# Performance work log

Hardware: AMD Instinct MI355X
Metric: run time of the kernel (lower is better)

The kernel has to match this reference:

```python
import jax, jax.numpy as jnp
import numpy as np

N_NODES = 30000
N_EDGES = 480000
N_GRAPHS = 500
D_IN = 78


def gcn_conv(x, W, b, src, dst, n_nodes):
    """PyG GCNConv: add self-loops, sym-normalize, linear then aggregate, bias after."""
    xw = x @ W  # [N, d_out]
    deg = jnp.zeros((n_nodes,), x.dtype).at[dst].add(1.0) + 1.0  # +1 self-loop
    dinv = jax.lax.rsqrt(deg)
    norm = dinv[src] * dinv[dst]  # [E]
    msg = xw[src] * norm[:, None]  # [E, d_out] edge gather
    out = jnp.zeros_like(xw).at[dst].add(msg)  # scatter-add to dst
    out = out + xw * (dinv * dinv)[:, None]  # self-loop contribution
    return out + b


def setup_inputs() -> dict:
    key = jax.random.key(0)
    ks = jax.random.split(key, 16)
    x = jax.random.normal(ks[0], (N_NODES, D_IN), dtype=jnp.float32)
    edge_index = jax.random.randint(ks[1], (2, N_EDGES), 0, N_NODES, dtype=jnp.int32)
    batch = jnp.sort(jax.random.randint(ks[2], (N_NODES,), 0, N_GRAPHS, dtype=jnp.int32))

    def lin(k, fi, fo):
        s = 1.0 / np.sqrt(fi)
        k1, k2 = jax.random.split(k)
        W = jax.random.uniform(k1, (fi, fo), jnp.float32, -s, s)
        b = jax.random.uniform(k2, (fo,), jnp.float32, -s, s)
        return W, b

    W1, b1 = lin(ks[3], D_IN, D_IN)
    W2, b2 = lin(ks[4], D_IN, D_IN * 2)
    W3, b3 = lin(ks[5], D_IN * 2, D_IN * 4)
    Wf1, bf1 = lin(ks[6], D_IN * 4, 1024)
    Wf2, bf2 = lin(ks[7], 1024, 128)
    return {"x": x, "edge_index": edge_index, "batch": batch,
            "W1": W1, "b1": b1, "W2": W2, "b2": b2, "W3": W3, "b3": b3,
            "Wf1": Wf1, "bf1": bf1, "Wf2": Wf2, "bf2": bf2}


def reference(x, edge_index, batch, W1, b1, W2, b2, W3, b3, Wf1, bf1, Wf2, bf2):
    src, dst = edge_index[0], edge_index[1]
    n = x.shape[0]
    h = jax.nn.relu(gcn_conv(x, W1, b1, src, dst, n))
    h = jax.nn.relu(gcn_conv(h, W2, b2, src, dst, n))
    h = jax.nn.relu(gcn_conv(h, W3, b3, src, dst, n))
    # global max pool over graphs
    pooled = jax.ops.segment_max(h, batch, num_segments=N_GRAPHS)  # [G, 312]
    pooled = jnp.where(jnp.isfinite(pooled), pooled, 0.0)  # guard empty segments
    out = jax.nn.relu(pooled @ Wf1 + bf1)
    out = out @ Wf2 + bf2  # dropout is identity in eval mode
    return out
```

## Files before the change

### kernel.cpp

```cpp
#include <hip/hip_runtime.h>

#define NODES  30000
#define EDGES  480000
#define GRAPHS 500
#define MPAD   30016
#define NB     118

typedef __bf16 bf16x8 __attribute__((ext_vector_type(8)));
typedef float  f32x4  __attribute__((ext_vector_type(4)));

__device__ __forceinline__ float4 f4add(float4 a, float4 b) {
    a.x += b.x; a.y += b.y; a.z += b.z; a.w += b.w; return a;
}
__device__ __forceinline__ float4 f4max(float4 a, float4 b) {
    a.x = fmaxf(a.x, b.x); a.y = fmaxf(a.y, b.y);
    a.z = fmaxf(a.z, b.z); a.w = fmaxf(a.w, b.w); return a;
}

__device__ __forceinline__ void split_f32(float a, unsigned short& hi, unsigned short& lo) {
    unsigned int u = __float_as_uint(a);
    unsigned int rh = (u + 0x7fffu + ((u >> 16) & 1u)) & 0xffff0000u;
    hi = (unsigned short)(rh >> 16);
    float l = a - __uint_as_float(rh);
    unsigned int ul = __float_as_uint(l);
    lo = (unsigned short)((ul + 0x7fffu + ((ul >> 16) & 1u)) >> 16);
}

__device__ __forceinline__ void gload_lds16(const void* g, void* l) {
    __builtin_amdgcn_global_load_lds(
        (__attribute__((address_space(1))) void*)g,
        (__attribute__((address_space(3))) void*)l, 16, 0, 0);
}

__global__ __launch_bounds__(256) void prep_kernel(
    const float* __restrict__ W1, const float* __restrict__ W2, const float* __restrict__ W3,
    unsigned short* __restrict__ h1, unsigned short* __restrict__ l1,
    unsigned short* __restrict__ h2, unsigned short* __restrict__ l2,
    unsigned short* __restrict__ h3, unsigned short* __restrict__ l3,
    const int* __restrict__ dst, int* __restrict__ cnt)
{
    int b = blockIdx.x, t = threadIdx.x;
    if (b < 640) {
        const float* W; unsigned short *oh, *ol; int n, K, N, Kp;
        if (b < 128)      { W = W1; oh = h1; ol = l1; n = b;       K = 78;  N = 78;  Kp = 96;  }
        else if (b < 320) { W = W2; oh = h2; ol = l2; n = b - 128; K = 78;  N = 156; Kp = 96;  }
        else              { W = W3; oh = h3; ol = l3; n = b - 320; K = 156; N = 312; Kp = 160; }
        if (t < Kp) {
            float v = (n < N && t < K) ? W[(size_t)t * N + n] : 0.0f;
            unsigned short h, l;
            split_f32(v, h, l);
            oh[(size_t)n * Kp + t] = h;
            ol[(size_t)n * Kp + t] = l;
        }
    } else {
        int i = (b - 640) * 256 + t;
        if (i < EDGES) atomicAdd(&cnt[dst[i]], 1);
    }
}

__global__ __launch_bounds__(256) void scan_bsum_kernel(const int* __restrict__ cnt,
                                                        int* __restrict__ bsum, int n) {
    __shared__ int buf[256];
    int t = threadIdx.x;
    int i = blockIdx.x * 256 + t;
    buf[t] = (i < n) ? cnt[i] : 0;
    __syncthreads();
    for (int ofs = 128; ofs > 0; ofs >>= 1) {
        if (t < ofs) buf[t] += buf[t + ofs];
        __syncthreads();
    }
    if (t == 0) bsum[blockIdx.x] = buf[0];
}

__global__ __launch_bounds__(128) void scan_top_kernel(const int* __restrict__ bsum,
                                                       int* __restrict__ boff) {
    __shared__ int buf[128];
    int t = threadIdx.x;
    int own = (t < NB) ? bsum[t] : 0;
    buf[t] = own;
    __syncthreads();
    for (int ofs = 1; ofs < 128; ofs <<= 1) {
        int v = (t >= ofs) ? buf[t - ofs] : 0;
        __syncthreads();
        buf[t] += v;
        __syncthreads();
    }
    if (t < NB) boff[t] = buf[t] - own;
}

__global__ __launch_bounds__(256) void scan_apply_kernel(const int* __restrict__ cnt,
                                                         const int* __restrict__ boff,
                                                         int* __restrict__ rowstart,
                                                         int* __restrict__ cursor,
                                                         float* __restrict__ dinv, int n) {
    __shared__ int buf[256];
    int t = threadIdx.x;
    int i = blockIdx.x * 256 + t;
    int own = (i < n) ? cnt[i] : 0;
    buf[t] = own;
    __syncthreads();
    for (int ofs = 1; ofs < 256; ofs <<= 1) {
        int v = (t >= ofs) ? buf[t - ofs] : 0;
        __syncthreads();
        buf[t] += v;
        __syncthreads();
    }
    if (i < n) {
        rowstart[i] = boff[blockIdx.x] + buf[t] - own;
        cursor[i] = 0;
        dinv[i] = rsqrtf((float)own + 1.0f);
    }
}

__global__ __launch_bounds__(256) void fill_prescale_kernel(
    const int* __restrict__ src, const int* __restrict__ dst,
    const int* __restrict__ rowstart, int* __restrict__ cursor, int* __restrict__ csr_src,
    const float* __restrict__ X, const float* __restrict__ dinv, float* __restrict__ Xs)
{
    int b = blockIdx.x, t = threadIdx.x;
    if (b < 1875) {
        int i = b * 256 + t;
        if (i < EDGES) {
            int d = dst[i];
            int pos = atomicAdd(&cursor[d], 1);
            csr_src[rowstart[d] + pos] = src[i];
        }
    } else {
        int i = (b - 1875) * 256 + t;
        if (i < NODES * 80) {
            int node = i / 80;
            int c = i - node * 80;
            Xs[i] = (c < 78) ? X[node * 78 + c] * dinv[node] : 0.0f;
        }
    }
}

template <int DV, int KQ>
__global__ __launch_bounds__(256) void agg_split_v4(
    const float* __restrict__ Xs, const int* __restrict__ rowstart,
    const int* __restrict__ cnt, const int* __restrict__ csr_src,
    const float* __restrict__ dinv,
    unsigned short* __restrict__ ohi, unsigned short* __restrict__ olo)
{
    constexpr int EPI = 64 / DV;
    constexpr int Kp = KQ * 4;
    int node = blockIdx.x * 4 + (threadIdx.x >> 6);
    int lane = threadIdx.x & 63;
    int sub = lane / DV;
    int c4 = lane - sub * DV;
    const float4* X4 = (const float4*)Xs;

    float4 accs[4] = {{0,0,0,0},{0,0,0,0},{0,0,0,0},{0,0,0,0}};
    int s = rowstart[node];
    int e = s + cnt[node];

    if (sub < EPI) {
        if (sub == 0) accs[0] = X4[(size_t)node * DV + c4];
        int j = s;
        for (; j + 12 * EPI <= e; j += 12 * EPI) {
            int idx[12];
            #pragma unroll
            for (int u = 0; u < 12; u++) idx[u] = csr_src[j + u * EPI + sub];
            float4 xv[12];
            #pragma unroll
            for (int u = 0; u < 12; u++) xv[u] = X4[(size_t)idx[u] * DV + c4];
            #pragma unroll
            for (int u = 0; u < 12; u++) accs[u & 3] = f4add(accs[u & 3], xv[u]);
        }
        for (; j + 4 * EPI <= e; j += 4 * EPI) {
            int idx[4];
            #pragma unroll
            for (int u = 0; u < 4; u++) idx[u] = csr_src[j + u * EPI + sub];
            float4 xv[4];
            #pragma unroll
            for (int u = 0; u < 4; u++) xv[u] = X4[(size_t)idx[u] * DV + c4];
            #pragma unroll
            for (int u = 0; u < 4; u++) accs[u] = f4add(accs[u], xv[u]);
        }
        for (; j < e; j += EPI) {
            int jj = j + sub;
            if (jj < e) {
                int idx = csr_src[jj];
                accs[0] = f4add(accs[0], X4[(size_t)idx * DV + c4]);
            }
        }
    }
    float4 acc = f4add(f4add(accs[0], accs[1]), f4add(accs[2], accs[3]));

    if constexpr (EPI > 1) {
        float sx[EPI - 1], sy[EPI - 1], sz[EPI - 1], sw[EPI - 1];
        #pragma unroll
        for (int sft = 1; sft < EPI; sft++) {
            sx[sft - 1] = __shfl(acc.x, lane + sft * DV);
            sy[sft - 1] = __shfl(acc.y, lane + sft * DV);
            sz[sft - 1] = __shfl(acc.z, lane + sft * DV);
            sw[sft - 1] = __shfl(acc.w, lane + sft * DV);
        }
        #pragma unroll
        for (int sft = 1; sft < EPI; sft++) {
            acc.x += sx[sft - 1];
            acc.y += sy[sft - 1];
            acc.z += sz[sft - 1];
            acc.w += sw[sft - 1];
        }
    }

    if (lane < KQ) {
        float di = (lane < DV) ? dinv[node] : 0.0f;
        ushort4 h4, l4;
        split_f32(acc.x * di, h4.x, l4.x);
        split_f32(acc.y * di, h4.y, l4.y);
        split_f32(acc.z * di, h4.z, l4.z);
        split_f32(acc.w * di, h4.w, l4.w);
        size_t off = (size_t)node * Kp + (size_t)lane * 4;
        *(ushort4*)&ohi[off] = h4;
        *(ushort4*)&olo[off] = l4;
    }
}

__global__ __launch_bounds__(256) void agg_split_h2(
    const float* __restrict__ Xs, const int* __restrict__ rowstart,
    const int* __restrict__ cnt, const int* __restrict__ csr_src,
    const float* __restrict__ dinv,
    unsigned short* __restrict__ ohi, unsigned short* __restrict__ olo)
{
    int node = blockIdx.x * 4 + (threadIdx.x >> 6);
    int lane = threadIdx.x & 63;
    int sub = lane / 20;
    int c4 = lane - sub * 20;
    const float4* X4 = (const float4*)Xs;

    float4 aA0 = {0,0,0,0}, aA1 = {0,0,0,0};
    float4 aB0 = {0,0,0,0}, aB1 = {0,0,0,0};
    int s = rowstart[node];
    int e = s + cnt[node];

    if (sub < 3) {
        if (sub == 0) {
            aA0 = X4[(size_t)node * 40 + c4];
            aB0 = X4[(size_t)node * 40 + 20 + c4];
        }
        int j = s;
        for (; j + 8 * 3 <= e; j += 8 * 3) {
            int idx[8];
            #pragma unroll
            for (int u = 0; u < 8; u++) idx[u] = csr_src[j + u * 3 + sub];
            float4 xa[8], xb[8];
            #pragma unroll
            for (int u = 0; u < 8; u++) {
                size_t base = (size_t)idx[u] * 40 + c4;
                xa[u] = X4[base];
                xb[u] = X4[base + 20];
            }
            #pragma unroll
            for (int u = 0; u < 8; u++) {
                if (u & 1) { aA1 = f4add(aA1, xa[u]); aB1 = f4add(aB1, xb[u]); }
                else       { aA0 = f4add(aA0, xa[u]); aB0 = f4add(aB0, xb[u]); }
            }
        }
        for (; j + 4 * 3 <= e; j += 4 * 3) {
            int idx[4];
            #pragma unroll
            for (int u = 0; u < 4; u++) idx[u] = csr_src[j + u * 3 + sub];
            float4 xa[4], xb[4];
            #pragma unroll
            for (int u = 0; u < 4; u++) {
                size_t base = (size_t)idx[u] * 40 + c4;
                xa[u] = X4[base];
                xb[u] = X4[base + 20];
            }
            #pragma unroll
            for (int u = 0; u < 4; u++) {
                if (u & 1) { aA1 = f4add(aA1, xa[u]); aB1 = f4add(aB1, xb[u]); }
                else       { aA0 = f4add(aA0, xa[u]); aB0 = f4add(aB0, xb[u]); }
            }
        }
        for (; j < e; j += 3) {
            int jj = j + sub;
            if (jj < e) {
                size_t base = (size_t)csr_src[jj] * 40 + c4;
                aA0 = f4add(aA0, X4[base]);
                aB0 = f4add(aB0, X4[base + 20]);
            }
        }
    }
    float4 accA = f4add(aA0, aA1);
    float4 accB = f4add(aB0, aB1);

    {
        float sx[2][2], sy[2][2], sz[2][2], sw[2][2];
        #pragma unroll
        for (int sft = 1; sft <= 2; sft++) {
            sx[sft - 1][0] = __shfl(accA.x, lane + sft * 20);
            sy[sft - 1][0] = __shfl(accA.y, lane + sft * 20);
            sz[sft - 1][0] = __shfl(accA.z, lane + sft * 20);
            sw[sft - 1][0] = __shfl(accA.w, lane + sft * 20);
            sx[sft - 1][1] = __shfl(accB.x, lane + sft * 20);
            sy[sft - 1][1] = __shfl(accB.y, lane + sft * 20);
            sz[sft - 1][1] = __shfl(accB.z, lane + sft * 20);
            sw[sft - 1][1] = __shfl(accB.w, lane + sft * 20);
        }
        #pragma unroll
        for (int sft = 1; sft <= 2; sft++) {
            accA.x += sx[sft - 1][0]; accA.y += sy[sft - 1][0];
            accA.z += sz[sft - 1][0]; accA.w += sw[sft - 1][0];
            accB.x += sx[sft - 1][1]; accB.y += sy[sft - 1][1];
            accB.z += sz[sft - 1][1]; accB.w += sw[sft - 1][1];
        }
    }

    if (lane < 20) {
        float di = dinv[node];
        ushort4 h4, l4;
        split_f32(accA.x * di, h4.x, l4.x);
        split_f32(accA.y * di, h4.y, l4.y);
        split_f32(accA.z * di, h4.z, l4.z);
        split_f32(accA.w * di, h4.w, l4.w);
        size_t off = (size_t)node * 160 + (size_t)lane * 4;
        *(ushort4*)&ohi[off] = h4;
        *(ushort4*)&olo[off] = l4;
        split_f32(accB.x * di, h4.x, l4.x);
        split_f32(accB.y * di, h4.y, l4.y);
        split_f32(accB.z * di, h4.z, l4.z);
        split_f32(accB.w * di, h4.w, l4.w);
        *(ushort4*)&ohi[off + 80] = h4;
        *(ushort4*)&olo[off + 80] = l4;
    }
}

template <int NCK>
__global__ __launch_bounds__(256) void mfma_gemm_v2(
    const unsigned short* __restrict__ Ahi, const unsigned short* __restrict__ Alo,
    const unsigned short* __restrict__ Bhi, const unsigned short* __restrict__ Blo,
    const float* __restrict__ bias, const float* __restrict__ scale,
    float* __restrict__ C, int M, int N, int Cstride, int nN, int do_relu)
{
    constexpr int Kp = NCK * 32;
    constexpr int CELLS = NCK * 256;
    extern __shared__ unsigned short smem[];
    unsigned short* sA = smem;
    unsigned short* sB = smem + 2 * CELLS * 8;

    int t = threadIdx.x;
    int wv = t >> 6, ln = t & 63;
    int q = ln >> 4, l16 = ln & 15;
    int wm = wv & 1, wn = wv >> 1;
    int m0 = blockIdx.x * 64;

    #pragma unroll
    for (int i = 0; i < 2 * NCK; i++) {
        int c = i * 256 + t;
        int plane = c / CELLS;
        int r = c - plane * CELLS;
        int ck = r >> 8, qq = (r >> 6) & 3, row = r & 63;
        const unsigned short* src = (plane ? Alo : Ahi) + (size_t)(m0 + row) * Kp + ck * 32 + qq * 8;
        gload_lds16(src, &sA[(size_t)c * 8]);
    }

    for (int nt = 0; nt < nN; nt++) {
        int n0 = nt * 64;
        if (nt > 0) __syncthreads();
        #pragma unroll
        for (int i = 0; i < 2 * NCK; i++) {
            int c = i * 256 + t;
            int plane = c / CELLS;
            int r = c - plane * CELLS;
            int ck = r >> 8, qq = (r >> 6) & 3, row = r & 63;
            const unsigned short* src = (plane ? Blo : Bhi) + (size_t)(n0 + row) * Kp + ck * 32 + qq * 8;
            gload_lds16(src, &sB[(size_t)c * 8]);
        }
        __syncthreads();

        f32x4 acc[2][2] = {};
        #pragma unroll
        for (int ck = 0; ck < NCK; ck++) {
            bf16x8 ah[2], al[2], bh[2], bl[2];
            #pragma unroll
            for (int i = 0; i < 2; i++) {
                int ra = wm * 32 + i * 16 + l16;
                int rb = wn * 32 + i * 16 + l16;
                ah[i] = *(const bf16x8*)&sA[(size_t)(((0 * NCK + ck) * 4 + q) * 64 + ra) * 8];
                al[i] = *(const bf16x8*)&sA[(size_t)(((1 * NCK + ck) * 4 + q) * 64 + ra) * 8];
                bh[i] = *(const bf16x8*)&sB[(size_t)(((0 * NCK + ck) * 4 + q) * 64 + rb) * 8];
                bl[i] = *(const bf16x8*)&sB[(size_t)(((1 * NCK + ck) * 4 + q) * 64 + rb) * 8];
            }
            #pragma unroll
            for (int i = 0; i < 2; i++)
                #pragma unroll
                for (int j = 0; j < 2; j++) {
                    acc[i][j] = __builtin_amdgcn_mfma_f32_16x16x32_bf16(ah[i], bh[j], acc[i][j], 0, 0, 0);
                    acc[i][j] = __builtin_amdgcn_mfma_f32_16x16x32_bf16(ah[i], bl[j], acc[i][j], 0, 0, 0);
                    acc[i][j] = __builtin_amdgcn_mfma_f32_16x16x32_bf16(al[i], bh[j], acc[i][j], 0, 0, 0);
                }
        }

        #pragma unroll
        for (int i = 0; i < 2; i++) {
            int rbase = m0 + wm * 32 + i * 16 + q * 4;
            #pragma unroll
            for (int j = 0; j < 2; j++) {
                int col = n0 + wn * 32 + j * 16 + l16;
                if (col >= Cstride) continue;
                float bv = (col < N) ? bias[col] : 0.0f;
                #pragma unroll
                for (int r = 0; r < 4; r++) {
                    int row = rbase + r;
                    if (row < M) {
                        float v = 0.0f;
                        if (col < N) {
                            v = acc[i][j][r] + bv;
                            if (do_relu) v = fmaxf(v, 0.0f);
                            if (scale) v *= scale[row];
                        }
                        C[(size_t)row * Cstride + col] = v;
                    }
                }
            }
        }
    }
}

__device__ inline int lower_bound_dev(const int* a, int n, int v) {
    int lo = 0, hi = n;
    while (lo < hi) { int mid = (lo + hi) >> 1; if (a[mid] < v) lo = mid + 1; else hi = mid; }
    return lo;
}

__global__ __launch_bounds__(256) void pool_kernel(const float* __restrict__ H,
                                                   const int* __restrict__ batch,
                                                   float* __restrict__ pooled, int n, int G) {
    __shared__ float4 red[3][78];
    int g = blockIdx.x;
    int t = threadIdx.x;
    int s = lower_bound_dev(batch, n, g);
    int e = lower_bound_dev(batch, n, g + 1);
    int rg = t / 78, c = t - rg * 78;
    const float4* H4 = (const float4*)H;
    if (rg < 3) {
        float4 m = {0.f, 0.f, 0.f, 0.f};
        for (int i = s + rg; i < e; i += 3)
            m = f4max(m, H4[(size_t)i * 78 + c]);
        red[rg][c] = m;
    }
    __syncthreads();
    if (t < 78) {
        float4 m = f4max(f4max(red[0][t], red[1][t]), red[2][t]);
        ((float4*)pooled)[(size_t)g * 78 + t] = m;
    }
}

__global__ __launch_bounds__(256) void fc1_kernel(const float* __restrict__ pooled,
                                                  const float* __restrict__ Wf1,
                                                  const float* __restrict__ bf1,
                                                  float* __restrict__ f1buf) {
    __shared__ float pl[4][312];
    int cb = blockIdx.x, gb = blockIdx.y;
    int t = threadIdx.x;
    for (int i = t; i < 4 * 312; i += 256) {
        int g = i / 312, k = i - g * 312;
        pl[g][k] = pooled[(size_t)(gb * 4 + g) * 312 + k];
    }
    __syncthreads();
    int col = cb * 256 + t;
    float a0 = 0.f, a1 = 0.f, a2 = 0.f, a3 = 0.f;
    #pragma unroll 4
    for (int k = 0; k < 312; k++) {
        float w = Wf1[(size_t)k * 1024 + col];
        a0 += pl[0][k] * w; a1 += pl[1][k] * w; a2 += pl[2][k] * w; a3 += pl[3][k] * w;
    }
    float b = bf1[col];
    int g0 = gb * 4;
    f1buf[(size_t)g0 * 1024 + col]       = fmaxf(a0 + b, 0.f);
    f1buf[(size_t)(g0 + 1) * 1024 + col] = fmaxf(a1 + b, 0.f);
    f1buf[(size_t)(g0 + 2) * 1024 + col] = fmaxf(a2 + b, 0.f);
    f1buf[(size_t)(g0 + 3) * 1024 + col] = fmaxf(a3 + b, 0.f);
}

__global__ __launch_bounds__(256) void fc2_part_kernel(const float* __restrict__ f1buf,
                                                       const float* __restrict__ Wf2,
                                                       float* __restrict__ partial) {
    __shared__ float f1s[4][128];
    __shared__ float red[256][4];
    int kt = blockIdx.x;
    int gb = blockIdx.y;
    int t = threadIdx.x;
    int col = t & 127, ks = t >> 7;
    for (int i = t; i < 512; i += 256) {
        int g = i >> 7, k = i & 127;
        f1s[g][k] = f1buf[(size_t)(gb * 4 + g) * 1024 + kt * 128 + k];
    }
    __syncthreads();
    float a0 = 0.f, a1 = 0.f, a2 = 0.f, a3 = 0.f;
    const float* w2 = Wf2 + (size_t)(kt * 128 + ks * 64) * 128 + col;
    #pragma unroll 4
    for (int k = 0; k < 64; k++) {
        float w = w2[(size_t)k * 128];
        int kk = ks * 64 + k;
        a0 += f1s[0][kk] * w; a1 += f1s[1][kk] * w; a2 += f1s[2][kk] * w; a3 += f1s[3][kk] * w;
    }
    red[t][0] = a0; red[t][1] = a1; red[t][2] = a2; red[t][3] = a3;
    __syncthreads();
    if (t < 128) {
        #pragma unroll
        for (int g = 0; g < 4; g++)
            partial[((size_t)kt * GRAPHS + gb * 4 + g) * 128 + col] = red[t][g] + red[t + 128][g];
    }
}

__global__ void fc2_reduce_kernel(const float* __restrict__ partial, const float* __restrict__ bf2,
                                  float* __restrict__ out, int total) {
    int i = blockIdx.x * blockDim.x + threadIdx.x;
    if (i < total) {
        float s = bf2[i & 127];
        #pragma unroll
        for (int kt = 0; kt < 8; kt++) s += partial[(size_t)kt * total + i];
        out[i] = s;
    }
}

extern "C" void kernel_launch(void* const* d_in, const int* in_sizes, int n_in,
                              void* d_out, int out_size, void* d_ws, size_t ws_size,
                              hipStream_t stream) {
    const float* x    = (const float*)d_in[0];
    const int*   ei   = (const int*)d_in[1];
    const int*   batch= (const int*)d_in[2];
    const float* W1 = (const float*)d_in[3];  const float* b1  = (const float*)d_in[4];
    const float* W2 = (const float*)d_in[5];  const float* b2  = (const float*)d_in[6];
    const float* W3 = (const float*)d_in[7];  const float* b3  = (const float*)d_in[8];
    const float* Wf1= (const float*)d_in[9];  const float* bf1 = (const float*)d_in[10];
    const float* Wf2= (const float*)d_in[11]; const float* bf2 = (const float*)d_in[12];
    float* out = (float*)d_out;

    const int* srcp = ei;
    const int* dstp = ei + EDGES;

    char* p = (char*)d_ws;
    size_t o = 0;
    auto takeB = [&](size_t bytes) { char* q = p + o; o += (bytes + 255) & ~(size_t)255; return q; };
    int*   cnt      = (int*)takeB(NODES * 4);
    int*   cursor   = (int*)takeB(NODES * 4);
    int*   rowstart = (int*)takeB(NODES * 4);
    int*   bsum     = (int*)takeB(NB * 4);
    int*   boff     = (int*)takeB(NB * 4);
    float* dinv     = (float*)takeB(NODES * 4);
    int*   csr_src  = (int*)takeB(EDGES * 4);
    unsigned short* aggH = (unsigned short*)takeB((size_t)MPAD * 160 * 2);
    unsigned short* aggL = (unsigned short*)takeB((size_t)MPAD * 160 * 2);
    float* xs      = (float*)takeB((size_t)NODES * 80 * 4);
    float* hbuf    = (float*)takeB((size_t)NODES * 312 * 4);
    float* pooled  = (float*)takeB((size_t)GRAPHS * 312 * 4);
    float* f1buf   = (float*)takeB((size_t)GRAPHS * 1024 * 4);
    float* partial = (float*)takeB((size_t)8 * GRAPHS * 128 * 4);
    unsigned short* Wt1h = (unsigned short*)takeB(128 * 96 * 2);
    unsigned short* Wt1l = (unsigned short*)takeB(128 * 96 * 2);
    unsigned short* Wt2h = (unsigned short*)takeB(192 * 96 * 2);
    unsigned short* Wt2l = (unsigned short*)takeB(192 * 96 * 2);
    unsigned short* Wt3h = (unsigned short*)takeB(320 * 160 * 2);
    unsigned short* Wt3l = (unsigned short*)takeB(320 * 160 * 2);
    (void)ws_size;

    hipMemsetAsync(cnt, 0, NODES * sizeof(int), stream);

    prep_kernel<<<640 + 1875, 256, 0, stream>>>(W1, W2, W3, Wt1h, Wt1l, Wt2h, Wt2l,
                                                Wt3h, Wt3l, dstp, cnt);
    scan_bsum_kernel<<<NB, 256, 0, stream>>>(cnt, bsum, NODES);
    scan_top_kernel<<<1, 128, 0, stream>>>(bsum, boff);
    scan_apply_kernel<<<NB, 256, 0, stream>>>(cnt, boff, rowstart, cursor, dinv, NODES);
    fill_prescale_kernel<<<1875 + 9375, 256, 0, stream>>>(srcp, dstp, rowstart, cursor,
                                                          csr_src, x, dinv, xs);

    const int NBLK = MPAD / 64;
    const int AGRID = NODES / 4;

    agg_split_v4<20, 24><<<AGRID, 256, 0, stream>>>(xs, rowstart, cnt, csr_src, dinv, aggH, aggL);
    mfma_gemm_v2<3><<<NBLK, 256, 3 * 16384, stream>>>(aggH, aggL, Wt1h, Wt1l, b1, dinv, hbuf,
                                                      NODES, 78, 80, 2, 1);
    agg_split_v4<20, 24><<<AGRID, 256, 0, stream>>>(hbuf, rowstart, cnt, csr_src, dinv, aggH, aggL);
    mfma_gemm_v2<3><<<NBLK, 256, 3 * 16384, stream>>>(aggH, aggL, Wt2h, Wt2l, b2, dinv, hbuf,
                                                      NODES, 156, 160, 3, 1);
    agg_split_h2<<<AGRID, 256, 0, stream>>>(hbuf, rowstart, cnt, csr_src, dinv, aggH, aggL);
    mfma_gemm_v2<5><<<NBLK, 256, 5 * 16384, stream>>>(aggH, aggL, Wt3h, Wt3l, b3, nullptr, hbuf,
                                                      NODES, 312, 312, 5, 1);

    pool_kernel<<<GRAPHS, 256, 0, stream>>>(hbuf, batch, pooled, NODES, GRAPHS);
    fc1_kernel<<<dim3(4, GRAPHS / 4), 256, 0, stream>>>(pooled, Wf1, bf1, f1buf);
    fc2_part_kernel<<<dim3(8, GRAPHS / 4), 256, 0, stream>>>(f1buf, Wf2, partial);
    fc2_reduce_kernel<<<(GRAPHS * 128 + 255) / 256, 256, 0, stream>>>(partial, bf2, out, GRAPHS * 128);
}
```

Before: 344.5 us.

## Store intermediate GCN features in fp16 to halve gather traffic in aggregation

The first two GEMMs now write their activations as fp16 instead of fp32. The layer-2 and layer-3 aggregation kernels are replaced by a templated fp16-gather kernel that reads 8 halves per lane and accumulates in fp32. This roughly halves the bytes moved by the random edge gathers, which dominate aggregation cost. The trade-off is reduced precision of the hidden activations before they are split into bf16 hi/lo pairs for the MFMA GEMM.

```diff
diff --git a/kernel.cpp b/kernel.cpp
--- a/kernel.cpp
+++ b/kernel.cpp
@@ -8,6 +8,8 @@
 
 typedef __bf16 bf16x8 __attribute__((ext_vector_type(8)));
 typedef float  f32x4  __attribute__((ext_vector_type(4)));
+typedef _Float16 half8v __attribute__((ext_vector_type(8)));
+typedef unsigned short ushort8v __attribute__((ext_vector_type(8)));
 
 __device__ __forceinline__ float4 f4add(float4 a, float4 b) {
     a.x += b.x; a.y += b.y; a.z += b.z; a.w += b.w; return a;
@@ -218,117 +220,93 @@
     }
 }
 
-__global__ __launch_bounds__(256) void agg_split_h2(
-    const float* __restrict__ Xs, const int* __restrict__ rowstart,
+template <int DVH, int KQH>
+__global__ __launch_bounds__(256) void agg_half(
+    const unsigned short* __restrict__ Xh, const int* __restrict__ rowstart,
     const int* __restrict__ cnt, const int* __restrict__ csr_src,
     const float* __restrict__ dinv,
     unsigned short* __restrict__ ohi, unsigned short* __restrict__ olo)
 {
+    constexpr int EPI = 64 / DVH;
+    constexpr int Kp = KQH * 8;
+    static_assert(EPI > 1, "EPI must exceed 1");
     int node = blockIdx.x * 4 + (threadIdx.x >> 6);
     int lane = threadIdx.x & 63;
-    int sub = lane / 20;
-    int c4 = lane - sub * 20;
-    const float4* X4 = (const float4*)Xs;
-
-    float4 aA0 = {0,0,0,0}, aA1 = {0,0,0,0};
-    float4 aB0 = {0,0,0,0}, aB1 = {0,0,0,0};
+    int sub = lane / DVH;
+    int c = lane - sub * DVH;
+    const half8v* X8 = (const half8v*)Xh;
+
+    float acc0[8] = {}, acc1[8] = {};
     int s = rowstart[node];
     int e = s + cnt[node];
 
-    if (sub < 3) {
+    if (sub < EPI) {
         if (sub == 0) {
-            aA0 = X4[(size_t)node * 40 + c4];
-            aB0 = X4[(size_t)node * 40 + 20 + c4];
+            half8v v = X8[(size_t)node * DVH + c];
+            #pragma unroll
+            for (int i = 0; i < 8; i++) acc0[i] += (float)v[i];
         }
         int j = s;
-        for (; j + 8 * 3 <= e; j += 8 * 3) {
-            int idx[8];
-            #pragma unroll
-            for (int u = 0; u < 8; u++) idx[u] = csr_src[j + u * 3 + sub];
-            float4 xa[8], xb[8];
-            #pragma unroll
-            for (int u = 0; u < 8; u++) {
-                size_t base = (size_t)idx[u] * 40 + c4;
-                xa[u] = X4[base];
-                xb[u] = X4[base + 20];
+        for (; j + 4 * EPI <= e; j += 4 * EPI) {
+            int i0 = csr_src[j + sub],           i1 = csr_src[j + EPI + sub];
+            int i2 = csr_src[j + 2 * EPI + sub], i3 = csr_src[j + 3 * EPI + sub];
+            half8v x0 = X8[(size_t)i0 * DVH + c], x1 = X8[(size_t)i1 * DVH + c];
+            half8v x2 = X8[(size_t)i2 * DVH + c], x3 = X8[(size_t)i3 * DVH + c];
+            #pragma unroll
+            for (int i = 0; i < 8; i++) {
+                acc0[i] += (float)x0[i] + (float)x2[i];
+                acc1[i] += (float)x1[i] + (float)x3[i];
             }
-            #pragma unroll
-            for (int u = 0; u < 8; u++) {
-                if (u & 1) { aA1 = f4add(aA1, xa[u]); aB1 = f4add(aB1, xb[u]); }
-                else       { aA0 = f4add(aA0, xa[u]); aB0 = f4add(aB0, xb[u]); }
-            }
-        }
-        for (; j + 4 * 3 <= e; j += 4 * 3) {
-            int idx[4];
-            #pragma unroll
-            for (int u = 0; u < 4; u++) idx[u] = csr_src[j + u * 3 + sub];
-            float4 xa[4], xb[4];
-            #pragma unroll
-            for (int u = 0; u < 4; u++) {
-                size_t base = (size_t)idx[u] * 40 + c4;
-                xa[u] = X4[base];
-                xb[u] = X4[base + 20];
-            }
-            #pragma unroll
-            for (int u = 0; u < 4; u++) {
-                if (u & 1) { aA1 = f4add(aA1, xa[u]); aB1 = f4add(aB1, xb[u]); }
-                else       { aA0 = f4add(aA0, xa[u]); aB0 = f4add(aB0, xb[u]); }
-            }
-        }
-        for (; j < e; j += 3) {
+        }
+        for (; j + 2 * EPI <= e; j += 2 * EPI) {
+            int i0 = csr_src[j + sub], i1 = csr_src[j + EPI + sub];
+            half8v x0 = X8[(size_t)i0 * DVH + c], x1 = X8[(size_t)i1 * DVH + c];
+            #pragma unroll
+            for (int i = 0; i < 8; i++) { acc0[i] += (float)x0[i]; acc1[i] += (float)x1[i]; }
+        }
+        for (; j < e; j += EPI) {
             int jj = j + sub;
             if (jj < e) {
-                size_t base = (size_t)csr_src[jj] * 40 + c4;
-                aA0 = f4add(aA0, X4[base]);
-                aB0 = f4add(aB0, X4[base + 20]);
+                half8v x = X8[(size_t)csr_src[jj] * DVH + c];
+                #pragma unroll
+                for (int i = 0; i < 8; i++) acc0[i] += (float)x[i];
             }
         }
     }
-    float4 accA = f4add(aA0, aA1);
-    float4 accB = f4add(aB0, aB1);
+    float acc[8];
+    #pragma unroll
+    for (int i = 0; i < 8; i++) acc[i] = acc0[i] + acc1[i];
 
     {
-        float sx[2][2], sy[2][2], sz[2][2], sw[2][2];
-        #pragma unroll
-        for (int sft = 1; sft <= 2; sft++) {
-            sx[sft - 1][0] = __shfl(accA.x, lane + sft * 20);
-            sy[sft - 1][0] = __shfl(accA.y, lane + sft * 20);
-            sz[sft - 1][0] = __shfl(accA.z, lane + sft * 20);
-            sw[sft - 1][0] = __shfl(accA.w, lane + sft * 20);
-            sx[sft - 1][1] = __shfl(accB.x, lane + sft * 20);
-            sy[sft - 1][1] = __shfl(accB.y, lane + sft * 20);
-            sz[sft - 1][1] = __shfl(accB.z, lane + sft * 20);
-            sw[sft - 1][1] = __shfl(accB.w, lane + sft * 20);
-        }
-        #pragma unroll
-        for (int sft = 1; sft <= 2; sft++) {
-            accA.x += sx[sft - 1][0]; accA.y += sy[sft - 1][0];
-            accA.z += sz[sft - 1][0]; accA.w += sw[sft - 1][0];
-            accB.x += sx[sft - 1][1]; accB.y += sy[sft - 1][1];
-            accB.z += sz[sft - 1][1]; accB.w += sw[sft - 1][1];
-        }
-    }
-
-    if (lane < 20) {
-        float di = dinv[node];
-        ushort4 h4, l4;
-        split_f32(accA.x * di, h4.x, l4.x);
-        split_f32(accA.y * di, h4.y, l4.y);
-        split_f32(accA.z * di, h4.z, l4.z);
-        split_f32(accA.w * di, h4.w, l4.w);
-        size_t off = (size_t)node * 160 + (size_t)lane * 4;
-        *(ushort4*)&ohi[off] = h4;
-        *(ushort4*)&olo[off] = l4;
-        split_f32(accB.x * di, h4.x, l4.x);
-        split_f32(accB.y * di, h4.y, l4.y);
-        split_f32(accB.z * di, h4.z, l4.z);
-        split_f32(accB.w * di, h4.w, l4.w);
-        *(ushort4*)&ohi[off + 80] = h4;
-        *(ushort4*)&olo[off + 80] = l4;
-    }
-}
-
-template <int NCK>
+        float tmp[EPI - 1][8];
+        #pragma unroll
+        for (int sft = 1; sft < EPI; sft++)
+            #pragma unroll
+            for (int i = 0; i < 8; i++)
+                tmp[sft - 1][i] = __shfl(acc[i], lane + sft * DVH);
+        #pragma unroll
+        for (int sft = 1; sft < EPI; sft++)
+            #pragma unroll
+            for (int i = 0; i < 8; i++)
+                acc[i] += tmp[sft - 1][i];
+    }
+
+    if (lane < KQH) {
+        float di = (lane < DVH) ? dinv[node] : 0.0f;
+        ushort8v h8, l8;
+        #pragma unroll
+        for (int i = 0; i < 8; i++) {
+            unsigned short hh, ll;
+            split_f32(acc[i] * di, hh, ll);
+            h8[i] = hh; l8[i] = ll;
+        }
+        size_t off = (size_t)node * Kp + (size_t)lane * 8;
+        *(ushort8v*)&ohi[off] = h8;
+        *(ushort8v*)&olo[off] = l8;
+    }
+}
+
+template <int NCK, int OUT16>
 __global__ __launch_bounds__(256) void mfma_gemm_v2(
     const unsigned short* __restrict__ Ahi, const unsigned short* __restrict__ Alo,
     const unsigned short* __restrict__ Bhi, const unsigned short* __restrict__ Blo,
@@ -412,7 +390,13 @@
                             if (do_relu) v = fmaxf(v, 0.0f);
                             if (scale) v *= scale[row];
                         }
-                        C[(size_t)row * Cstride + col] = v;
+                        if constexpr (OUT16) {
+                            _Float16 hv = (_Float16)v;
+                            ((unsigned short*)C)[(size_t)row * Cstride + col] =
+                                __builtin_bit_cast(unsigned short, hv);
+                        } else {
+                            C[(size_t)row * Cstride + col] = v;
+                        }
                     }
                 }
             }
@@ -548,6 +532,8 @@
     unsigned short* aggL = (unsigned short*)takeB((size_t)MPAD * 160 * 2);
     float* xs      = (float*)takeB((size_t)NODES * 80 * 4);
     float* hbuf    = (float*)takeB((size_t)NODES * 312 * 4);
+    unsigned short* h16_1 = (unsigned short*)takeB((size_t)MPAD * 80 * 2);
+    unsigned short* h16_2 = (unsigned short*)takeB((size_t)MPAD * 160 * 2);
     float* pooled  = (float*)takeB((size_t)GRAPHS * 312 * 4);
     float* f1buf   = (float*)takeB((size_t)GRAPHS * 1024 * 4);
     float* partial = (float*)takeB((size_t)8 * GRAPHS * 128 * 4);
@@ -573,14 +559,14 @@
     const int AGRID = NODES / 4;
 
     agg_split_v4<20, 24><<<AGRID, 256, 0, stream>>>(xs, rowstart, cnt, csr_src, dinv, aggH, aggL);
-    mfma_gemm_v2<3><<<NBLK, 256, 3 * 16384, stream>>>(aggH, aggL, Wt1h, Wt1l, b1, dinv, hbuf,
-                                                      NODES, 78, 80, 2, 1);
-    agg_split_v4<20, 24><<<AGRID, 256, 0, stream>>>(hbuf, rowstart, cnt, csr_src, dinv, aggH, aggL);
-    mfma_gemm_v2<3><<<NBLK, 256, 3 * 16384, stream>>>(aggH, aggL, Wt2h, Wt2l, b2, dinv, hbuf,
-                                                      NODES, 156, 160, 3, 1);
-    agg_split_h2<<<AGRID, 256, 0, stream>>>(hbuf, rowstart, cnt, csr_src, dinv, aggH, aggL);
-    mfma_gemm_v2<5><<<NBLK, 256, 5 * 16384, stream>>>(aggH, aggL, Wt3h, Wt3l, b3, nullptr, hbuf,
-                                                      NODES, 312, 312, 5, 1);
+    mfma_gemm_v2<3, 1><<<NBLK, 256, 3 * 16384, stream>>>(aggH, aggL, Wt1h, Wt1l, b1, dinv,
+                                                         (float*)h16_1, NODES, 78, 80, 2, 1);
+    agg_half<10, 12><<<AGRID, 256, 0, stream>>>(h16_1, rowstart, cnt, csr_src, dinv, aggH, aggL);
+    mfma_gemm_v2<3, 1><<<NBLK, 256, 3 * 16384, stream>>>(aggH, aggL, Wt2h, Wt2l, b2, dinv,
+                                                         (float*)h16_2, NODES, 156, 160, 3, 1);
+    agg_half<20, 20><<<AGRID, 256, 0, stream>>>(h16_2, rowstart, cnt, csr_src, dinv, aggH, aggL);
+    mfma_gemm_v2<5, 0><<<NBLK, 256, 5 * 16384, stream>>>(aggH, aggL, Wt3h, Wt3l, b3, nullptr,
+                                                         hbuf, NODES, 312, 312, 5, 1);
 
     pool_kernel<<<GRAPHS, 256, 0, stream>>>(hbuf, batch, pooled, NODES, GRAPHS);
     fc1_kernel<<<dim3(4, GRAPHS / 4), 256, 0, stream>>>(pooled, Wf1, bf1, f1buf);
```

Measured after the change: 320.2 us. -7.1%, faster.
